# Performance work log

Measured on AMD Instinct MI355X. Metric: run time of the kernel, lower is better.

The kernel has to match this reference:

```python
import jax, jax.numpy as jnp
import numpy as np

ND, PD, NH = 256, 128, 8   # node_dim, pair_dim, n_head
HD = ND // NH              # head_dim = 32
N, L = 1, 256


def _inorm(x):
    # InstanceNorm2d (affine=False), x is NHWC: normalize per (N,C) over H,W
    m = jnp.mean(x, axis=(1, 2), keepdims=True)
    v = jnp.var(x, axis=(1, 2), keepdims=True)
    return (x - m) * jax.lax.rsqrt(v + 1e-5)


def _conv3x3(x, w, b):
    # w in torch OIHW layout -> HWIO; stride 1, padding 1 ('SAME')
    y = jax.lax.conv_general_dilated(x, jnp.transpose(w, (2, 3, 1, 0)), (1, 1), 'SAME',
                                     dimension_numbers=('NHWC', 'HWIO', 'NHWC'))
    return y + b


def _lrelu(x):
    return jnp.where(x >= 0, x, 0.01 * x)


def _ln(x, g, b):
    m = jnp.mean(x, axis=-1, keepdims=True)
    v = jnp.var(x, axis=-1, keepdims=True)
    return (x - m) * jax.lax.rsqrt(v + 1e-5) * g + b


def setup_inputs() -> dict:
    key = jax.random.key(0)
    ks = jax.random.split(key, 16)
    rn = lambda k, s: jax.random.normal(k, s, jnp.float32) * 0.02
    return dict(
        x=jax.random.normal(ks[0], (N, L, ND), jnp.float32),
        z=jax.random.normal(ks[1], (N, L, L, PD), jnp.float32),
        plddt=jax.random.uniform(ks[2], (N, L, L, 1), jnp.float32),
        Wq=rn(ks[3], (ND, ND)), Wk=rn(ks[4], (ND, ND)), Wv=rn(ks[5], (ND, ND)),
        Wp2a=rn(ks[6], (NH, PD)),
        conv_a_w=rn(ks[7], (NH, 2 * NH, 3, 3)), conv_a_b=jnp.zeros((NH,), jnp.float32),
        conv_p_w=rn(ks[8], (NH, NH + 1, 3, 3)), conv_p_b=jnp.zeros((NH,), jnp.float32),
        ln1_g=jnp.ones((NH * PD + ND,), jnp.float32), ln1_b=jnp.zeros((NH * PD + ND,), jnp.float32),
        lin1_w=rn(ks[9], (2 * ND, NH * PD + ND)), lin1_b=jnp.zeros((2 * ND,), jnp.float32),
        ln2_g=jnp.ones((2 * ND,), jnp.float32), ln2_b=jnp.zeros((2 * ND,), jnp.float32),
        lin2_w=rn(ks[10], (ND, 2 * ND)), lin2_b=jnp.zeros((ND,), jnp.float32),
        lnf_g=jnp.ones((ND,), jnp.float32), lnf_b=jnp.zeros((ND,), jnp.float32),
        conv_z_w=rn(ks[11], (PD, NH + PD, 3, 3)), conv_z_b=jnp.zeros((PD,), jnp.float32),
    )


def reference(x, z, plddt, Wq, Wk, Wv, Wp2a, conv_a_w, conv_a_b, conv_p_w, conv_p_b,
              ln1_g, ln1_b, lin1_w, lin1_b, ln2_g, ln2_b, lin2_w, lin2_b,
              lnf_g, lnf_b, conv_z_w, conv_z_b):
    n, l, _ = x.shape
    inv_sqrt_hd = np.float32(1.0 / np.sqrt(HD))
    # _node2alpha: per-head QK^T / sqrt(head_dim) -> (N,L,L,H)
    q = (x @ Wq.T).reshape(n, l, NH, HD)
    k = (x @ Wk.T).reshape(n, l, NH, HD)
    v = (x @ Wv.T).reshape(n, l, NH, HD)
    a_node = jnp.einsum('nihd,njhd->nijh', q, k) * inv_sqrt_hd
    # _pair2alpha
    a_pair = z @ Wp2a.T  # (N,L,L,H)
    # conv2dalpha: cat(pair, node) channels-last, InstanceNorm + Conv3x3 + LeakyReLU
    alpha = _lrelu(_conv3x3(_inorm(jnp.concatenate([a_pair, a_node], axis=-1)), conv_a_w, conv_a_b))
    # alpha_mask_plddt
    alpha = _lrelu(_conv3x3(_inorm(jnp.concatenate([alpha, plddt], axis=-1)), conv_p_w, conv_p_b))
    # _node_aggregation: (N,L,H,hd) head-major flatten -> (N,L,node_dim)
    node_from_node = jnp.einsum('nijh,njhd->nihd', alpha, v).reshape(n, l, ND)
    # _pair_aggregation: direct contraction over j (avoids (N,L,L,H,P) blowup)
    node_from_pair = jnp.einsum('nijh,nijp->nihp', alpha, z).reshape(n, l, NH * PD)
    # out_transform: LN -> Linear -> LN -> LeakyReLU -> Linear
    h = jnp.concatenate([node_from_pair, node_from_node], axis=-1)
    h = _ln(h, ln1_g, ln1_b)
    h = _ln(h @ lin1_w.T + lin1_b, ln2_g, ln2_b)
    x_out = _lrelu(h) @ lin2_w.T + lin2_b
    x_new = _ln(x + x_out, lnf_g, lnf_b)
    # alpha2pair
    z_new = _lrelu(_conv3x3(_inorm(jnp.concatenate([z, alpha], axis=-1)), conv_z_w, conv_z_b))
    return x_new, z_new
```

## Files before the change

kernel.cpp:

```cpp
#include <hip/hip_runtime.h>
#include <math.h>

#define LLEN 256
#define NDIM 256
#define NHEAD 8
#define HDIM 32
#define NPIX (LLEN*LLEN)

typedef __bf16 bf16x8 __attribute__((ext_vector_type(8)));
typedef float f32x4 __attribute__((ext_vector_type(4)));

constexpr size_t OFF_Q     = 0;
constexpr size_t OFF_K     = 65536;
constexpr size_t OFF_V     = 131072;
constexpr size_t OFF_CAT16 = 196608;
constexpr size_t OFF_H1B   = 196608;
constexpr size_t OFF_W1B   = 360448;
constexpr size_t OFF_A1    = 1245184;
constexpr size_t OFF_ALPHA = 1769472;
constexpr size_t OFF_AGG   = 2293760;
constexpr size_t OFF_Y     = 2621440;
constexpr size_t OFF_ST16  = 2752512;
constexpr size_t OFF_ST9   = 2752544;
constexpr size_t OFF_ST136 = 2752576;
constexpr size_t OFF_PART  = 2752864;
constexpr size_t OFF_PART2 = 2892128;
constexpr size_t OFF_WZB2  = 3031392;

__device__ inline unsigned short f2b(float x){
  union { float f; unsigned u; } a; a.f = x;
  unsigned r = a.u + 0x7fffu + ((a.u >> 16) & 1u);
  return (unsigned short)(r >> 16);
}

__global__ __launch_bounds__(256) void qkv2_kernel(
    const float* __restrict__ x, const float* __restrict__ Wq,
    const float* __restrict__ Wk, const float* __restrict__ Wv,
    float* __restrict__ q, float* __restrict__ k, float* __restrict__ v){
  __shared__ __align__(16) float xs[4][256];
  int t = threadIdx.x;
  int i0 = blockIdx.x * 4;
  int m = blockIdx.y;
  const float* W = (m==0)?Wq:((m==1)?Wk:Wv);
  float* out = (m==0)?q:((m==1)?k:v);
  for (int idx = t; idx < 1024; idx += 256)
    xs[idx>>8][idx&255] = x[(size_t)i0*256 + idx];
  __syncthreads();
  float acc[4];
  #pragma unroll
  for (int r = 0; r < 4; r++) acc[r] = 0.f;
  const float4* wr = (const float4*)(W + (size_t)t*256);
  for (int kk = 0; kk < 64; ++kk){
    float4 w4 = wr[kk];
    #pragma unroll
    for (int r = 0; r < 4; r++){
      float4 xv = ((const float4*)xs[r])[kk];
      acc[r] += w4.x*xv.x + w4.y*xv.y + w4.z*xv.z + w4.w*xv.w;
    }
  }
  #pragma unroll
  for (int r = 0; r < 4; r++) out[(size_t)(i0+r)*256 + t] = acc[r];
}

__global__ __launch_bounds__(256) void cat16v4_kernel(
    const float* __restrict__ z, const float* __restrict__ qb,
    const float* __restrict__ kb, const float* __restrict__ Wp2a,
    float* __restrict__ cat16, float* __restrict__ p16, float* __restrict__ p16q){
  __shared__ __align__(16) float zs2[32*132];
  __shared__ __align__(16) float ws2[8*132];
  __shared__ float sA[512];
  int t = threadIdx.x;
  int pix0 = blockIdx.x * 32;
  int i = pix0 >> 8;
  int j0 = pix0 & 255;
  { int h = t >> 5, j = t & 31;
    float4 v = *(const float4*)(Wp2a + h*128 + j*4);
    *(float4*)(ws2 + h*132 + j*4) = v; }
  #pragma unroll
  for (int k = 0; k < 4; ++k){
    int idx = t + k*256;
    int pix = idx >> 5, j = idx & 31;
    float4 v = *(const float4*)(z + ((size_t)(pix0 + pix))*128 + j*4);
    *(float4*)(zs2 + pix*132 + j*4) = v;
  }
  __syncthreads();
  int p8 = t >> 3, h = t & 7;
  const float* zr = zs2 + p8*132;
  const float* wr = ws2 + h*132;
  float ap = 0.f;
  #pragma unroll 8
  for (int j = 0; j < 32; ++j){
    float4 a = *(const float4*)(zr + j*4);
    float4 b = *(const float4*)(wr + j*4);
    ap += a.x*b.x + a.y*b.y + a.z*b.z + a.w*b.w;
  }
  const float* qg = qb + (size_t)i*256 + h*32;
  const float* kg = kb + (size_t)(j0 + p8)*256 + h*32;
  float an = 0.f;
  #pragma unroll
  for (int d4 = 0; d4 < 8; ++d4){
    float4 a = *(const float4*)(qg + d4*4);
    float4 b = *(const float4*)(kg + d4*4);
    an += a.x*b.x + a.y*b.y + a.z*b.z + a.w*b.w;
  }
  an *= 0.17677669529663689f;
  int pix = pix0 + p8;
  cat16[(size_t)pix*16 + h] = ap;
  cat16[(size_t)pix*16 + 8 + h] = an;
  sA[p8*16 + h] = ap;
  sA[p8*16 + 8 + h] = an;
  __syncthreads();
  if (t < 16){
    float S = 0.f, Q = 0.f;
    #pragma unroll
    for (int p = 0; p < 32; ++p){ float v = sA[p*16 + t]; S += v; Q += v*v; }
    p16 [(size_t)t*2048 + blockIdx.x] = S;
    p16q[(size_t)t*2048 + blockIdx.x] = Q;
  }
}

__global__ __launch_bounds__(256) void statsA_z_kernel(
    const float* __restrict__ z, float* __restrict__ part, float* __restrict__ part2){
  __shared__ float4 sm[256], sq[256];
  int t = threadIdx.x, b = blockIdx.x;
  int c4 = t & 31, po = t >> 5;
  float4 s = {0,0,0,0}, q = {0,0,0,0};
  for (int g = 0; g < 8; ++g){
    int px = b*64 + po + g*8;
    float4 v = *(const float4*)(z + (size_t)px*128 + c4*4);
    s.x += v.x; s.y += v.y; s.z += v.z; s.w += v.w;
    q.x += v.x*v.x; q.y += v.y*v.y; q.z += v.z*v.z; q.w += v.w*v.w;
  }
  sm[t] = s; sq[t] = q;
  __syncthreads();
  if (t < 32){
    float4 S = sm[t], Q = sq[t];
    for (int p2 = 1; p2 < 8; ++p2){
      float4 a = sm[p2*32 + t], c = sq[p2*32 + t];
      S.x += a.x; S.y += a.y; S.z += a.z; S.w += a.w;
      Q.x += c.x; Q.y += c.y; Q.z += c.z; Q.w += c.w;
    }
    part [(size_t)(t*4+0)*1024 + b] = S.x; part [(size_t)(t*4+1)*1024 + b] = S.y;
    part [(size_t)(t*4+2)*1024 + b] = S.z; part [(size_t)(t*4+3)*1024 + b] = S.w;
    part2[(size_t)(t*4+0)*1024 + b] = Q.x; part2[(size_t)(t*4+1)*1024 + b] = Q.y;
    part2[(size_t)(t*4+2)*1024 + b] = Q.z; part2[(size_t)(t*4+3)*1024 + b] = Q.w;
  }
}

__device__ inline void block_reduce2(float& s, float& s2, float* red){
  int t = threadIdx.x;
  int lane = t & 63, wv = t >> 6;
  #pragma unroll
  for (int o = 32; o > 0; o >>= 1){ s += __shfl_down(s, o); s2 += __shfl_down(s2, o); }
  __syncthreads();
  if (lane == 0){ red[wv] = s; red[4+wv] = s2; }
  __syncthreads();
  s  = red[0]+red[1]+red[2]+red[3];
  s2 = red[4]+red[5]+red[6]+red[7];
}

__global__ __launch_bounds__(256) void statsB_kernel(
    const float* __restrict__ part, const float* __restrict__ part2,
    float* __restrict__ st, int C, int nb, int stride){
  __shared__ float red[8];
  int c = blockIdx.x, t = threadIdx.x;
  float s = 0.f, q = 0.f;
  for (int i = t; i < nb; i += 256){
    s += part[(size_t)c*stride + i];
    q += part2[(size_t)c*stride + i];
  }
  block_reduce2(s, q, red);
  if (t == 0){
    float m = s * (1.f/NPIX);
    float var = q * (1.f/NPIX) - m*m;
    st[c] = m;
    st[C + c] = rsqrtf(var + 1e-5f);
  }
}

template<int CIN, int COUT, bool PL>
__global__ __launch_bounds__(256) void conv_small6_kernel(
    const float* __restrict__ A, int Ca, const float* __restrict__ B, int Cb,
    const float* __restrict__ st, const float* __restrict__ w,
    const float* __restrict__ bias, float* __restrict__ out,
    const float* __restrict__ plddt, float* __restrict__ part,
    float* __restrict__ part2, int coff){
  constexpr int WD = 67;
  __shared__ float xn[3][CIN][WD];
  __shared__ float wsm[COUT*CIN*9];
  __shared__ float ms[CIN], isd[CIN], bs[COUT];
  __shared__ float sB[COUT*64];
  __shared__ float sP[64];
  int t = threadIdx.x;
  int i = blockIdx.x >> 2, chb = blockIdx.x & 3;
  int c0 = chb*64;
  if (t < CIN){ ms[t] = st[t]; isd[t] = st[CIN + t]; }
  if (t < COUT) bs[t] = bias[t];
  for (int idx = t; idx < COUT*CIN*9; idx += 256) wsm[idx] = w[idx];
  __syncthreads();
  constexpr int TOT = 66*CIN;
  for (int s = 0; s < 3; ++s){
    int ir = i - 1 + s;
    for (int idx = t; idx < TOT; idx += 256){
      int col = idx / CIN, c = idx - col*CIN;
      int gcol = c0 + col - 1;
      float vv = 0.f;
      if (ir >= 0 && ir < 256 && gcol >= 0 && gcol < 256){
        size_t pix = (size_t)ir*256 + gcol;
        float raw = (c < Ca) ? A[pix*Ca + c] : B[pix*Cb + (c - Ca)];
        vv = (raw - ms[c]) * isd[c];
      }
      xn[s][c][col] = vv;
    }
  }
  __syncthreads();
  int os = t >> 6, tc = t & 63;
  float a0 = bs[os*2], a1 = bs[os*2 + 1];
  #pragma unroll
  for (int kh = 0; kh < 3; ++kh){
    #pragma unroll
    for (int c = 0; c < CIN; ++c){
      float x0 = xn[kh][c][tc];
      float x1 = xn[kh][c][tc + 1];
      float x2 = xn[kh][c][tc + 2];
      const float* w0 = wsm + (((os*2+0)*CIN + c)*3 + kh)*3;
      const float* w1 = wsm + (((os*2+1)*CIN + c)*3 + kh)*3;
      a0 += x0*w0[0] + x1*w0[1] + x2*w0[2];
      a1 += x0*w1[0] + x1*w1[1] + x2*w1[2];
    }
  }
  a0 = (a0 >= 0.f) ? a0 : 0.01f*a0;
  a1 = (a1 >= 0.f) ? a1 : 0.01f*a1;
  float2 v2 = { a0, a1 };
  *(float2*)(out + ((size_t)(i*256 + c0 + tc))*COUT + os*2) = v2;
  sB[os*128 + tc]      = a0;
  sB[os*128 + 64 + tc] = a1;
  if (PL && t < 64) sP[t] = plddt[(size_t)i*256 + c0 + t];
  __syncthreads();
  if (t < COUT){
    int os2 = t >> 1, par = t & 1;
    const float* src = sB + os2*128 + par*64;
    float S = 0.f, Q = 0.f;
    #pragma unroll
    for (int j = 0; j < 64; ++j){ float v = src[j]; S += v; Q += v*v; }
    part [(size_t)(coff + t)*1024 + blockIdx.x] = S;
    part2[(size_t)(coff + t)*1024 + blockIdx.x] = Q;
  } else if (PL && t == COUT){
    float S = 0.f, Q = 0.f;
    #pragma unroll
    for (int j = 0; j < 64; ++j){ float v = sP[j]; S += v; Q += v*v; }
    part [(size_t)(coff + COUT)*1024 + blockIdx.x] = S;
    part2[(size_t)(coff + COUT)*1024 + blockIdx.x] = Q;
  }
}

__global__ __launch_bounds__(512) void agg_kernel2(
    const float* __restrict__ alpha, const float* __restrict__ z,
    const float* __restrict__ v, float* __restrict__ agg){
  __shared__ float as[2048];
  __shared__ float pp[256][4];
  __shared__ float np[256];
  int i = blockIdx.x, t = threadIdx.x;
  for (int idx = t; idx < 2048; idx += 512) as[idx] = alpha[(size_t)i*2048 + idx];
  __syncthreads();
  int tt = t & 255, jh = t >> 8;
  int p = tt & 127, hh = tt >> 7;
  const float* zrow = z + (size_t)i*32768 + (size_t)jh*128*128;
  const float* ar0 = as + jh*128*8;
  float a0=0.f, a1=0.f, a2=0.f, a3=0.f;
  #pragma unroll 8
  for (int j = 0; j < 128; ++j){
    float zv = zrow[j*128 + p];
    const float* ar = ar0 + j*8 + hh*4;
    a0 += ar[0]*zv; a1 += ar[1]*zv; a2 += ar[2]*zv; a3 += ar[3]*zv;
  }
  int h = tt >> 5;
  float an = 0.f;
  const float* vrow = v + (size_t)jh*128*256;
  const float* ah0 = as + jh*128*8;
  #pragma unroll 8
  for (int j = 0; j < 128; ++j) an += ah0[j*8 + h]*vrow[j*256 + tt];
  if (jh == 1){
    pp[tt][0]=a0; pp[tt][1]=a1; pp[tt][2]=a2; pp[tt][3]=a3; np[tt]=an;
  }
  __syncthreads();
  if (jh == 0){
    a0 += pp[tt][0]; a1 += pp[tt][1]; a2 += pp[tt][2]; a3 += pp[tt][3];
    an += np[tt];
    size_t ob = (size_t)i*1280;
    agg[ob + (hh*4+0)*128 + p] = a0;
    agg[ob + (hh*4+1)*128 + p] = a1;
    agg[ob + (hh*4+2)*128 + p] = a2;
    agg[ob + (hh*4+3)*128 + p] = a3;
    agg[ob + 1024 + tt] = an;
  }
}

__global__ __launch_bounds__(256) void ln1_kernel(
    const float* __restrict__ agg,
    const float* __restrict__ ln1_g, const float* __restrict__ ln1_b,
    unsigned short* __restrict__ h1b){
  __shared__ float red[8];
  int i = blockIdx.x, t = threadIdx.x;
  float v[5], s = 0.f, s2 = 0.f;
  #pragma unroll
  for (int qq = 0; qq < 5; ++qq){
    v[qq] = agg[(size_t)i*1280 + qq*256 + t];
    s += v[qq]; s2 += v[qq]*v[qq];
  }
  block_reduce2(s, s2, red);
  float m = s*(1.f/1280.f), istd = rsqrtf(s2*(1.f/1280.f) - m*m + 1e-5f);
  #pragma unroll
  for (int qq = 0; qq < 5; ++qq){
    int kk = qq*256 + t;
    h1b[(size_t)i*1280 + kk] = f2b((v[qq] - m)*istd*ln1_g[kk] + ln1_b[kk]);
  }
}

__global__ __launch_bounds__(256) void w1_prep(const float* __restrict__ w,
                                               unsigned short* __restrict__ wb){
  int idx = (blockIdx.x*256 + threadIdx.x)*4;
  float4 v = *(const float4*)(w + idx);
  ushort4 u;
  u.x = f2b(v.x); u.y = f2b(v.y); u.z = f2b(v.z); u.w = f2b(v.w);
  *(ushort4*)(wb + idx) = u;
}

__global__ __launch_bounds__(256) void gemm1_kernel(
    const unsigned short* __restrict__ h1b, const unsigned short* __restrict__ w1b,
    const float* __restrict__ lin1_b, float* __restrict__ y){
  int t = threadIdx.x;
  int mb = blockIdx.x & 3, nb = blockIdx.x >> 2;
  int lane = t & 63, w = t >> 6;
  int li = lane & 15, lg = lane >> 4;
  int mh = w & 1, nh = w >> 1;
  int mbase = mb*64 + mh*32, nbase = nb*64 + nh*32;
  f32x4 acc[2][2];
  #pragma unroll
  for (int a = 0; a < 2; ++a)
    #pragma unroll
    for (int b = 0; b < 2; ++b) acc[a][b] = (f32x4){0.f,0.f,0.f,0.f};
  const unsigned short* ar0 = h1b + (size_t)(mbase + li)*1280 + lg*8;
  const unsigned short* ar1 = ar0 + 16*1280;
  const unsigned short* br0 = w1b + (size_t)(nbase + li)*1280 + lg*8;
  const unsigned short* br1 = br0 + 16*1280;
  #pragma unroll 4
  for (int ks = 0; ks < 40; ++ks){
    bf16x8 a0 = *(const bf16x8*)(ar0 + ks*32);
    bf16x8 a1 = *(const bf16x8*)(ar1 + ks*32);
    bf16x8 b0 = *(const bf16x8*)(br0 + ks*32);
    bf16x8 b1 = *(const bf16x8*)(br1 + ks*32);
    acc[0][0] = __builtin_amdgcn_mfma_f32_16x16x32_bf16(a0, b0, acc[0][0], 0,0,0);
    acc[0][1] = __builtin_amdgcn_mfma_f32_16x16x32_bf16(a0, b1, acc[0][1], 0,0,0);
    acc[1][0] = __builtin_amdgcn_mfma_f32_16x16x32_bf16(a1, b0, acc[1][0], 0,0,0);
    acc[1][1] = __builtin_amdgcn_mfma_f32_16x16x32_bf16(a1, b1, acc[1][1], 0,0,0);
  }
  #pragma unroll
  for (int mi = 0; mi < 2; ++mi){
    #pragma unroll
    for (int ni = 0; ni < 2; ++ni){
      int col = nbase + ni*16 + li;
      float bb = lin1_b[col];
      #pragma unroll
      for (int ri = 0; ri < 4; ++ri){
        int row = mbase + mi*16 + lg*4 + ri;
        y[(size_t)row*512 + col] = acc[mi][ni][ri] + bb;
      }
    }
  }
}

__global__ __launch_bounds__(256) void outB2_kernel(
    const float* __restrict__ y, const float* __restrict__ x,
    const float* __restrict__ ln2_g, const float* __restrict__ ln2_b,
    const float* __restrict__ lin2_w, const float* __restrict__ lin2_b,
    const float* __restrict__ lnf_g, const float* __restrict__ lnf_b,
    float* __restrict__ xout){
  __shared__ __align__(16) float h2[2][512];
  __shared__ float red[8];
  int t = threadIdx.x;
  int rb = blockIdx.x;
  for (int r = 0; r < 2; ++r){
    int i = rb*2 + r;
    float y0 = y[(size_t)i*512 + t], y1 = y[(size_t)i*512 + 256 + t];
    float s = y0 + y1, s2 = y0*y0 + y1*y1;
    block_reduce2(s, s2, red);
    float m = s*(1.f/512.f), istd = rsqrtf(s2*(1.f/512.f) - m*m + 1e-5f);
    float z0 = (y0 - m)*istd*ln2_g[t] + ln2_b[t];
    float z1 = (y1 - m)*istd*ln2_g[t+256] + ln2_b[t+256];
    h2[r][t]     = (z0 >= 0.f) ? z0 : 0.01f*z0;
    h2[r][t+256] = (z1 >= 0.f) ? z1 : 0.01f*z1;
  }
  __syncthreads();
  float acc[2];
  acc[0] = 0.f; acc[1] = 0.f;
  const float4* wr = (const float4*)(lin2_w + (size_t)t*512);
  #pragma unroll 4
  for (int kk = 0; kk < 128; ++kk){
    float4 w4 = wr[kk];
    #pragma unroll
    for (int r = 0; r < 2; ++r){
      float4 h = ((const float4*)h2[r])[kk];
      acc[r] += w4.x*h.x + w4.y*h.y + w4.z*h.z + w4.w*h.w;
    }
  }
  float bb = lin2_b[t];
  for (int r = 0; r < 2; ++r){
    int i = rb*2 + r;
    float xr = x[(size_t)i*256 + t] + acc[r] + bb;
    float s = xr, s2 = xr*xr;
    block_reduce2(s, s2, red);
    float m = s*(1.f/256.f), istd = rsqrtf(s2*(1.f/256.f) - m*m + 1e-5f);
    xout[(size_t)i*256 + t] = (xr - m)*istd*lnf_g[t] + lnf_b[t];
  }
}

__global__ __launch_bounds__(256) void wz_prep2(const float* __restrict__ w,
                                                unsigned short* __restrict__ wzb2){
  int idx = blockIdx.x*256 + threadIdx.x;
  if (idx >= 23040) return;
  int lane = idx & 63;
  int f = idx >> 6;
  int k = f % 5; int ft = f / 5; int tap = ft % 9; int ocb = ft / 9;
  int oc = ocb*16 + (lane & 15);
  int chb = k*32 + (lane >> 4)*8;
  unsigned short u[8];
  #pragma unroll
  for (int j = 0; j < 8; ++j){
    int ch = chb + j;
    float vv = (ch < 136) ? w[(size_t)oc*1224 + ch*9 + tap] : 0.f;
    u[j] = f2b(vv);
  }
  uint4 pk;
  pk.x = (unsigned)u[0] | ((unsigned)u[1]<<16);
  pk.y = (unsigned)u[2] | ((unsigned)u[3]<<16);
  pk.z = (unsigned)u[4] | ((unsigned)u[5]<<16);
  pk.w = (unsigned)u[6] | ((unsigned)u[7]<<16);
  *(uint4*)(wzb2 + (size_t)idx*8) = pk;
}

__global__ __launch_bounds__(256) void conv_z7_kernel(
    const float* __restrict__ z, const float* __restrict__ alpha,
    const float* __restrict__ st, const unsigned short* __restrict__ wzb2,
    const float* __restrict__ bias, float* __restrict__ out){
  __shared__ __align__(16) unsigned short xs[4*578*8];
  __shared__ float msp[153], isp[153];
  int t = threadIdx.x;
  int stripe = blockIdx.x & 7, rg = blockIdx.x >> 3;
  int i0 = rg*2, c0 = stripe*32;
  int lane = t & 63, w = t >> 6;
  int li = lane & 15, lg = lane >> 4;
  int wocb = w*2;
  if (t < 153){
    int cq = t/9, j = t - cq*9;
    bool vld = (j < 8);
    int ch = cq*8 + j;
    msp[t] = vld ? st[ch] : 0.f;
    isp[t] = vld ? st[136 + ch] : 0.f;
  }
  __syncthreads();
  for (int it = 0; it < 3; ++it){
    int cidx = t + it*256;
    int col = cidx / 17, cq = cidx - col*17;
    int gcol = c0 + col - 1;
    float mm[8], ss[8];
    #pragma unroll
    for (int j = 0; j < 8; ++j){ mm[j] = msp[cq*9 + j]; ss[j] = isp[cq*9 + j]; }
    if (cidx < 578){
      #pragma unroll
      for (int s = 0; s < 4; ++s){
        int ir = i0 - 1 + s;
        uint4 pk = {0u,0u,0u,0u};
        if (ir >= 0 && ir < 256 && gcol >= 0 && gcol < 256){
          const float* src = (cq < 16) ? (z + ((size_t)ir*256 + gcol)*128 + cq*8)
                                       : (alpha + ((size_t)ir*256 + gcol)*8);
          float4 r0 = *(const float4*)src;
          float4 r1 = *(const float4*)(src + 4);
          unsigned short u0 = f2b((r0.x - mm[0])*ss[0]);
          unsigned short u1 = f2b((r0.y - mm[1])*ss[1]);
          unsigned short u2 = f2b((r0.z - mm[2])*ss[2]);
          unsigned short u3 = f2b((r0.w - mm[3])*ss[3]);
          unsigned short u4 = f2b((r1.x - mm[4])*ss[4]);
          unsigned short u5 = f2b((r1.y - mm[5])*ss[5]);
          unsigned short u6 = f2b((r1.z - mm[6])*ss[6]);
          unsigned short u7 = f2b((r1.w - mm[7])*ss[7]);
          pk.x = (unsigned)u0 | ((unsigned)u1<<16);
          pk.y = (unsigned)u2 | ((unsigned)u3<<16);
          pk.z = (unsigned)u4 | ((unsigned)u5<<16);
          pk.w = (unsigned)u6 | ((unsigned)u7<<16);
        }
        *(uint4*)(xs + ((size_t)(s*578 + cidx))*8) = pk;
      }
    }
  }
  __syncthreads();

  f32x4 acc[2][2][2];
  #pragma unroll
  for (int r = 0; r < 2; ++r)
    #pragma unroll
    for (int m = 0; m < 2; ++m)
      #pragma unroll
      for (int o = 0; o < 2; ++o) acc[r][m][o] = (f32x4){0.f,0.f,0.f,0.f};

  for (int kh = 0; kh < 3; ++kh){
    for (int kw = 0; kw < 3; ++kw){
      int tap = kh*3 + kw;
      bf16x8 wf[5][2];
      #pragma unroll
      for (int k = 0; k < 5; ++k)
        #pragma unroll
        for (int o = 0; o < 2; ++o)
          wf[k][o] = *(const bf16x8*)(wzb2 + (size_t)((((wocb+o)*9 + tap)*5 + k)*64 + lane)*8);
      #pragma unroll
      for (int r = 0; r < 2; ++r){
        const unsigned short* sb = xs + (size_t)(r + kh)*578*8;
        #pragma unroll
        for (int k = 0; k < 5; ++k){
          int cq = (k < 4) ? (k*4 + lg) : 16;
          bf16x8 a0 = *(const bf16x8*)(sb + ((li+kw)*17 + cq)*8);
          bf16x8 a1 = *(const bf16x8*)(sb + ((li+kw+16)*17 + cq)*8);
          acc[r][0][0] = __builtin_amdgcn_mfma_f32_16x16x32_bf16(a0, wf[k][0], acc[r][0][0], 0,0,0);
          acc[r][0][1] = __builtin_amdgcn_mfma_f32_16x16x32_bf16(a0, wf[k][1], acc[r][0][1], 0,0,0);
          acc[r][1][0] = __builtin_amdgcn_mfma_f32_16x16x32_bf16(a1, wf[k][0], acc[r][1][0], 0,0,0);
          acc[r][1][1] = __builtin_amdgcn_mfma_f32_16x16x32_bf16(a1, wf[k][1], acc[r][1][1], 0,0,0);
        }
      }
    }
  }

  float b0 = bias[wocb*16 + li];
  float b1 = bias[(wocb+1)*16 + li];
  #pragma unroll
  for (int r = 0; r < 2; ++r){
    int i = i0 + r;
    #pragma unroll
    for (int m = 0; m < 2; ++m){
      #pragma unroll
      for (int ri = 0; ri < 4; ++ri){
        int px = m*16 + lg*4 + ri;
        size_t obase = ((size_t)(i*256 + c0 + px))*128;
        float v0 = acc[r][m][0][ri] + b0;
        float v1 = acc[r][m][1][ri] + b1;
        v0 = (v0 >= 0.f) ? v0 : 0.01f*v0;
        v1 = (v1 >= 0.f) ? v1 : 0.01f*v1;
        out[obase + wocb*16 + li]     = v0;
        out[obase + (wocb+1)*16 + li] = v1;
      }
    }
  }
}

extern "C" void kernel_launch(void* const* d_in, const int* in_sizes, int n_in,
                              void* d_out, int out_size, void* d_ws, size_t ws_size,
                              hipStream_t stream){
  const float* x        = (const float*)d_in[0];
  const float* z        = (const float*)d_in[1];
  const float* plddt    = (const float*)d_in[2];
  const float* Wq       = (const float*)d_in[3];
  const float* Wk       = (const float*)d_in[4];
  const float* Wv       = (const float*)d_in[5];
  const float* Wp2a     = (const float*)d_in[6];
  const float* conv_a_w = (const float*)d_in[7];
  const float* conv_a_b = (const float*)d_in[8];
  const float* conv_p_w = (const float*)d_in[9];
  const float* conv_p_b = (const float*)d_in[10];
  const float* ln1_g    = (const float*)d_in[11];
  const float* ln1_b    = (const float*)d_in[12];
  const float* lin1_w   = (const float*)d_in[13];
  const float* lin1_b   = (const float*)d_in[14];
  const float* ln2_g    = (const float*)d_in[15];
  const float* ln2_b    = (const float*)d_in[16];
  const float* lin2_w   = (const float*)d_in[17];
  const float* lin2_b   = (const float*)d_in[18];
  const float* lnf_g    = (const float*)d_in[19];
  const float* lnf_b    = (const float*)d_in[20];
  const float* conv_z_w = (const float*)d_in[21];
  const float* conv_z_b = (const float*)d_in[22];

  float* ws    = (float*)d_ws;
  float* q     = ws + OFF_Q;
  float* k     = ws + OFF_K;
  float* v     = ws + OFF_V;
  float* cat16 = ws + OFF_CAT16;
  float* a1    = ws + OFF_A1;
  float* alpha = ws + OFF_ALPHA;
  float* agg   = ws + OFF_AGG;
  float* y     = ws + OFF_Y;
  float* p16   = ws + OFF_Y;
  float* p16q  = ws + OFF_Y + 32768;
  float* st16  = ws + OFF_ST16;
  float* st9   = ws + OFF_ST9;
  float* st136 = ws + OFF_ST136;
  float* part  = ws + OFF_PART;
  float* part2 = ws + OFF_PART2;
  unsigned short* wzb2 = (unsigned short*)(ws + OFF_WZB2);
  unsigned short* h1b  = (unsigned short*)(ws + OFF_H1B);
  unsigned short* w1b  = (unsigned short*)(ws + OFF_W1B);

  float* xout = (float*)d_out;
  float* zout = (float*)d_out + 65536;

  qkv2_kernel<<<dim3(64,3), 256, 0, stream>>>(x, Wq, Wk, Wv, q, k, v);
  cat16v4_kernel<<<2048, 256, 0, stream>>>(z, q, k, Wp2a, cat16, p16, p16q);
  statsB_kernel<<<16, 256, 0, stream>>>(p16, p16q, st16, 16, 2048, 2048);
  conv_small6_kernel<16,8,true><<<1024, 256, 0, stream>>>(
      cat16, 16, (const float*)nullptr, 0, st16, conv_a_w, conv_a_b, a1,
      plddt, part, part2, 0);
  statsB_kernel<<<9, 256, 0, stream>>>(part, part2, st9, 9, 1024, 1024);
  conv_small6_kernel<9,8,false><<<1024, 256, 0, stream>>>(
      a1, 8, plddt, 1, st9, conv_p_w, conv_p_b, alpha,
      (const float*)nullptr, part, part2, 128);
  agg_kernel2<<<256, 512, 0, stream>>>(alpha, z, v, agg);
  w1_prep<<<640, 256, 0, stream>>>(lin1_w, w1b);
  ln1_kernel<<<256, 256, 0, stream>>>(agg, ln1_g, ln1_b, h1b);
  gemm1_kernel<<<32, 256, 0, stream>>>(h1b, w1b, lin1_b, y);
  outB2_kernel<<<128, 256, 0, stream>>>(y, x, ln2_g, ln2_b, lin2_w, lin2_b,
                                        lnf_g, lnf_b, xout);
  statsA_z_kernel<<<1024, 256, 0, stream>>>(z, part, part2);
  statsB_kernel<<<136, 256, 0, stream>>>(part, part2, st136, 136, 1024, 1024);
  wz_prep2<<<90, 256, 0, stream>>>(conv_z_w, wzb2);
  conv_z7_kernel<<<1024, 256, 0, stream>>>(z, alpha, st136, wzb2, conv_z_b, zout);
}
```

Baseline: 182.0 us.

## Fold z channel statistics into cat16 pass and merge weight prep kernels

The per-channel sum and sum-of-squares of z are now computed inside the cat16 kernel from the z tile already staged in shared memory. This removes the separate statsA_z pass, which read all of z a second time. The alpha-channel statistics for the final instance norm are reduced from the partials the second small conv already writes, using a new offset parameter on statsB. The two weight-conversion kernels are merged into a single launch. Together these remove roughly 32 MB of extra z traffic and two kernel launches, at the cost of more partial-sum buffers and an extra small stats launch.

```diff
diff --git a/kernel.cpp b/kernel.cpp
--- a/kernel.cpp
+++ b/kernel.cpp
@@ -62,10 +62,11 @@
   for (int r = 0; r < 4; r++) out[(size_t)(i0+r)*256 + t] = acc[r];
 }
 
-__global__ __launch_bounds__(256) void cat16v4_kernel(
+__global__ __launch_bounds__(256) void cat16v5_kernel(
     const float* __restrict__ z, const float* __restrict__ qb,
     const float* __restrict__ kb, const float* __restrict__ Wp2a,
-    float* __restrict__ cat16, float* __restrict__ p16, float* __restrict__ p16q){
+    float* __restrict__ cat16, float* __restrict__ p16, float* __restrict__ p16q,
+    float* __restrict__ zpart, float* __restrict__ zpartq){
   __shared__ __align__(16) float zs2[32*132];
   __shared__ __align__(16) float ws2[8*132];
   __shared__ float sA[512];
@@ -117,33 +118,12 @@
     p16 [(size_t)t*2048 + blockIdx.x] = S;
     p16q[(size_t)t*2048 + blockIdx.x] = Q;
   }
-}
-
-__global__ __launch_bounds__(256) void statsA_z_kernel(
-    const float* __restrict__ z, float* __restrict__ part, float* __restrict__ part2){
-  __shared__ float4 sm[256], sq[256];
-  int t = threadIdx.x, b = blockIdx.x;
-  int c4 = t & 31, po = t >> 5;
-  float4 s = {0,0,0,0}, q = {0,0,0,0};
-  for (int g = 0; g < 8; ++g){
-    int px = b*64 + po + g*8;
-    float4 v = *(const float4*)(z + (size_t)px*128 + c4*4);
-    s.x += v.x; s.y += v.y; s.z += v.z; s.w += v.w;
-    q.x += v.x*v.x; q.y += v.y*v.y; q.z += v.z*v.z; q.w += v.w*v.w;
-  }
-  sm[t] = s; sq[t] = q;
-  __syncthreads();
-  if (t < 32){
-    float4 S = sm[t], Q = sq[t];
-    for (int p2 = 1; p2 < 8; ++p2){
-      float4 a = sm[p2*32 + t], c = sq[p2*32 + t];
-      S.x += a.x; S.y += a.y; S.z += a.z; S.w += a.w;
-      Q.x += c.x; Q.y += c.y; Q.z += c.z; Q.w += c.w;
-    }
-    part [(size_t)(t*4+0)*1024 + b] = S.x; part [(size_t)(t*4+1)*1024 + b] = S.y;
-    part [(size_t)(t*4+2)*1024 + b] = S.z; part [(size_t)(t*4+3)*1024 + b] = S.w;
-    part2[(size_t)(t*4+0)*1024 + b] = Q.x; part2[(size_t)(t*4+1)*1024 + b] = Q.y;
-    part2[(size_t)(t*4+2)*1024 + b] = Q.z; part2[(size_t)(t*4+3)*1024 + b] = Q.w;
+  if (t < 128){
+    float S = 0.f, Q = 0.f;
+    #pragma unroll 8
+    for (int p = 0; p < 32; ++p){ float v = zs2[p*132 + t]; S += v; Q += v*v; }
+    zpart [(size_t)t*2048 + blockIdx.x] = S;
+    zpartq[(size_t)t*2048 + blockIdx.x] = Q;
   }
 }
 
@@ -161,7 +141,7 @@
 
 __global__ __launch_bounds__(256) void statsB_kernel(
     const float* __restrict__ part, const float* __restrict__ part2,
-    float* __restrict__ st, int C, int nb, int stride){
+    float* __restrict__ st, int C, int co, int nb, int stride){
   __shared__ float red[8];
   int c = blockIdx.x, t = threadIdx.x;
   float s = 0.f, q = 0.f;
@@ -173,8 +153,8 @@
   if (t == 0){
     float m = s * (1.f/NPIX);
     float var = q * (1.f/NPIX) - m*m;
-    st[c] = m;
-    st[C + c] = rsqrtf(var + 1e-5f);
+    st[co + c] = m;
+    st[C + co + c] = rsqrtf(var + 1e-5f);
   }
 }
 
@@ -317,13 +297,39 @@
   }
 }
 
-__global__ __launch_bounds__(256) void w1_prep(const float* __restrict__ w,
-                                               unsigned short* __restrict__ wb){
-  int idx = (blockIdx.x*256 + threadIdx.x)*4;
-  float4 v = *(const float4*)(w + idx);
-  ushort4 u;
-  u.x = f2b(v.x); u.y = f2b(v.y); u.z = f2b(v.z); u.w = f2b(v.w);
-  *(ushort4*)(wb + idx) = u;
+__global__ __launch_bounds__(256) void prep_kernel(
+    const float* __restrict__ lw, unsigned short* __restrict__ wb,
+    const float* __restrict__ zw, unsigned short* __restrict__ wzb2){
+  int bid = blockIdx.x;
+  if (bid < 640){
+    int idx = (bid*256 + threadIdx.x)*4;
+    float4 v = *(const float4*)(lw + idx);
+    ushort4 u;
+    u.x = f2b(v.x); u.y = f2b(v.y); u.z = f2b(v.z); u.w = f2b(v.w);
+    *(ushort4*)(wb + idx) = u;
+  } else {
+    int idx = (bid - 640)*256 + threadIdx.x;
+    if (idx < 23040){
+      int lane = idx & 63;
+      int f = idx >> 6;
+      int k = f % 5; int ft = f / 5; int tap = ft % 9; int ocb = ft / 9;
+      int oc = ocb*16 + (lane & 15);
+      int chb = k*32 + (lane >> 4)*8;
+      unsigned short u[8];
+      #pragma unroll
+      for (int j = 0; j < 8; ++j){
+        int ch = chb + j;
+        float vv = (ch < 136) ? zw[(size_t)oc*1224 + ch*9 + tap] : 0.f;
+        u[j] = f2b(vv);
+      }
+      uint4 pk;
+      pk.x = (unsigned)u[0] | ((unsigned)u[1]<<16);
+      pk.y = (unsigned)u[2] | ((unsigned)u[3]<<16);
+      pk.z = (unsigned)u[4] | ((unsigned)u[5]<<16);
+      pk.w = (unsigned)u[6] | ((unsigned)u[7]<<16);
+      *(uint4*)(wzb2 + (size_t)idx*8) = pk;
+    }
+  }
 }
 
 __global__ __launch_bounds__(256) void gemm1_kernel(
@@ -413,30 +419,6 @@
     float m = s*(1.f/256.f), istd = rsqrtf(s2*(1.f/256.f) - m*m + 1e-5f);
     xout[(size_t)i*256 + t] = (xr - m)*istd*lnf_g[t] + lnf_b[t];
   }
-}
-
-__global__ __launch_bounds__(256) void wz_prep2(const float* __restrict__ w,
-                                                unsigned short* __restrict__ wzb2){
-  int idx = blockIdx.x*256 + threadIdx.x;
-  if (idx >= 23040) return;
-  int lane = idx & 63;
-  int f = idx >> 6;
-  int k = f % 5; int ft = f / 5; int tap = ft % 9; int ocb = ft / 9;
-  int oc = ocb*16 + (lane & 15);
-  int chb = k*32 + (lane >> 4)*8;
-  unsigned short u[8];
-  #pragma unroll
-  for (int j = 0; j < 8; ++j){
-    int ch = chb + j;
-    float vv = (ch < 136) ? w[(size_t)oc*1224 + ch*9 + tap] : 0.f;
-    u[j] = f2b(vv);
-  }
-  uint4 pk;
-  pk.x = (unsigned)u[0] | ((unsigned)u[1]<<16);
-  pk.y = (unsigned)u[2] | ((unsigned)u[3]<<16);
-  pk.z = (unsigned)u[4] | ((unsigned)u[5]<<16);
-  pk.w = (unsigned)u[6] | ((unsigned)u[7]<<16);
-  *(uint4*)(wzb2 + (size_t)idx*8) = pk;
 }
 
 __global__ __launch_bounds__(256) void conv_z7_kernel(
@@ -584,6 +566,8 @@
   float* v     = ws + OFF_V;
   float* cat16 = ws + OFF_CAT16;
   float* a1    = ws + OFF_A1;
+  float* zpart = ws + OFF_A1;
+  float* zpartq= ws + OFF_A1 + 262144;
   float* alpha = ws + OFF_ALPHA;
   float* agg   = ws + OFF_AGG;
   float* y     = ws + OFF_Y;
@@ -602,23 +586,25 @@
   float* zout = (float*)d_out + 65536;
 
   qkv2_kernel<<<dim3(64,3), 256, 0, stream>>>(x, Wq, Wk, Wv, q, k, v);
-  cat16v4_kernel<<<2048, 256, 0, stream>>>(z, q, k, Wp2a, cat16, p16, p16q);
-  statsB_kernel<<<16, 256, 0, stream>>>(p16, p16q, st16, 16, 2048, 2048);
+  cat16v5_kernel<<<2048, 256, 0, stream>>>(z, q, k, Wp2a, cat16, p16, p16q,
+                                           zpart, zpartq);
+  statsB_kernel<<<16, 256, 0, stream>>>(p16, p16q, st16, 16, 0, 2048, 2048);
+  statsB_kernel<<<128, 256, 0, stream>>>(zpart, zpartq, st136, 136, 0, 2048, 2048);
   conv_small6_kernel<16,8,true><<<1024, 256, 0, stream>>>(
       cat16, 16, (const float*)nullptr, 0, st16, conv_a_w, conv_a_b, a1,
       plddt, part, part2, 0);
-  statsB_kernel<<<9, 256, 0, stream>>>(part, part2, st9, 9, 1024, 1024);
+  statsB_kernel<<<9, 256, 0, stream>>>(part, part2, st9, 9, 0, 1024, 1024);
   conv_small6_kernel<9,8,false><<<1024, 256, 0, stream>>>(
       a1, 8, plddt, 1, st9, conv_p_w, conv_p_b, alpha,
       (const float*)nullptr, part, part2, 128);
+  statsB_kernel<<<8, 256, 0, stream>>>(part + (size_t)128*1024,
+                                       part2 + (size_t)128*1024,
+                                       st136, 136, 128, 1024, 1024);
   agg_kernel2<<<256, 512, 0, stream>>>(alpha, z, v, agg);
-  w1_prep<<<640, 256, 0, stream>>>(lin1_w, w1b);
+  prep_kernel<<<730, 256, 0, stream>>>(lin1_w, w1b, conv_z_w, wzb2);
   ln1_kernel<<<256, 256, 0, stream>>>(agg, ln1_g, ln1_b, h1b);
   gemm1_kernel<<<32, 256, 0, stream>>>(h1b, w1b, lin1_b, y);
   outB2_kernel<<<128, 256, 0, stream>>>(y, x, ln2_g, ln2_b, lin2_w, lin2_b,
                                         lnf_g, lnf_b, xout);
-  statsA_z_kernel<<<1024, 256, 0, stream>>>(z, part, part2);
-  statsB_kernel<<<136, 256, 0, stream>>>(part, part2, st136, 136, 1024, 1024);
-  wz_prep2<<<90, 256, 0, stream>>>(conv_z_w, wzb2);
   conv_z7_kernel<<<1024, 256, 0, stream>>>(z, alpha, st136, wzb2, conv_z_b, zout);
 }
```

New measurement: 180.5 us. Within noise of the previous version (-0.8%).
